# Kernel tuning notes

Hardware: AMD Instinct MI355X
Metric: run time of the kernel (lower is better)

The kernel has to match this reference:

```python
import jax, jax.numpy as jnp
import numpy as np

N = 12288   # nodes
E = 393216  # edges (avg degree 32)
D = 128     # input feature dim


def setup_inputs() -> dict:
    key = jax.random.key(0)
    ks = jax.random.split(key, 8)
    x = jax.random.normal(ks[0], (N, D), dtype=jnp.float32)
    edge_index = jax.random.randint(ks[1], (2, E), 0, N, dtype=jnp.int64)
    def glorot(k, fan_in, fan_out):
        s = jnp.sqrt(6.0 / (fan_in + fan_out)).astype(jnp.float32)
        return jax.random.uniform(k, (fan_in, fan_out), jnp.float32, -s, s)
    W1 = glorot(ks[2], D, 16);  b1 = jnp.zeros((16,), jnp.float32)
    W2 = glorot(ks[3], 16, 8);  b2 = jnp.zeros((8,), jnp.float32)
    Wa = glorot(ks[4], 8, D);   ba = jnp.zeros((D,), jnp.float32)
    Ws = glorot(ks[5], 8, 8);   bs = jnp.zeros((8,), jnp.float32)
    return {"x": x, "edge_index": edge_index,
            "W1": W1, "b1": b1, "W2": W2, "b2": b2,
            "Wa": Wa, "ba": ba, "Ws": Ws, "bs": bs}


def reference(x, edge_index, W1, b1, W2, b2, Wa, ba, Ws, bs):
    n = x.shape[0]
    # GCN symmetric normalization with self-loops (PyG GCNConv defaults)
    loops = jnp.arange(n, dtype=edge_index.dtype)
    src = jnp.concatenate([edge_index[0], loops])
    dst = jnp.concatenate([edge_index[1], loops])
    deg = jax.ops.segment_sum(jnp.ones_like(dst, dtype=x.dtype), dst, num_segments=n)
    dinv = jnp.where(deg > 0, jax.lax.rsqrt(deg), 0.0)
    norm = dinv[src] * dinv[dst]  # [E+N]

    def gcn(h, W, b):
        h = h @ W                                   # [n, out]
        msg = h[src] * norm[:, None]                # gather + scale
        return jax.ops.segment_sum(msg, dst, num_segments=n) + b

    z = jax.nn.relu(gcn(x, W1, b1))
    z = jax.nn.relu(gcn(z, W2, b2))
    x_hat = gcn(z, Wa, ba)
    z_struct = jax.nn.relu(gcn(z, Ws, bs))
    a_hat = z_struct @ z_struct.T                   # [n, n] inner-product decoder
    return (x_hat, a_hat)
```

## Files before the change

kernel.cpp:

```cpp
#include <hip/hip_runtime.h>

typedef float f32x4 __attribute__((ext_vector_type(4)));

#define TPB 256
#define CAP 96

__global__ __launch_bounds__(256) void p1_kernel(
        const float* __restrict__ x, const float* __restrict__ W1,
        const int* __restrict__ src, const int* __restrict__ dst,
        int* __restrict__ cnt, unsigned short* __restrict__ csrd,
        float* __restrict__ h1, int n, int e, int nsb) {
    if ((int)blockIdx.x < nsb) {
        int t = blockIdx.x * blockDim.x + threadIdx.x;
        if (t < e) {
            int d = dst[t];
            int slot = atomicAdd(&cnt[d], 1);
            if (slot < CAP) csrd[(size_t)d * CAP + slot] = (unsigned short)src[t];
        }
        return;
    }
    __shared__ float sW[2048];
    for (int t = threadIdx.x; t < 2048; t += blockDim.x) sW[t] = W1[t];
    __syncthreads();
    int t = ((int)blockIdx.x - nsb) * blockDim.x + threadIdx.x;
    if (t >= n * 16) return;
    int i = t >> 4, j = t & 15;
    const float* xr = x + (size_t)i * 128;
    float s = 0.f;
#pragma unroll
    for (int k = 0; k < 128; k += 4) {
        f32x4 xv = *reinterpret_cast<const f32x4*>(xr + k);
        s = fmaf(xv.x, sW[(k + 0) * 16 + j], s);
        s = fmaf(xv.y, sW[(k + 1) * 16 + j], s);
        s = fmaf(xv.z, sW[(k + 2) * 16 + j], s);
        s = fmaf(xv.w, sW[(k + 3) * 16 + j], s);
    }
    h1[t] = s;
}

__global__ __launch_bounds__(256) void gather_l1(
        const float* __restrict__ h1, const int* __restrict__ cnt,
        const unsigned short* __restrict__ csrd,
        const float* __restrict__ b1, const float* __restrict__ W2,
        float* __restrict__ h2, int n) {
    int wave = (blockIdx.x * blockDim.x + threadIdx.x) >> 6;
    int lane = threadIdx.x & 63;
    if (wave >= n) return;
    const int i = wave;
    const int c = lane & 15;
    const int eg = lane >> 4;
    const unsigned short* row = csrd + (size_t)i * CAP;
    int cn = cnt[i];
    int deg = min(cn, CAP);
    float acc = 0.0f;
    for (int eb = eg; eb < deg; eb += 4) {
        int s = row[eb];
        float ds = rsqrtf((float)(cnt[s] + 1));
        acc = fmaf(ds, h1[(size_t)s * 16 + c], acc);
    }
    acc += __shfl_xor(acc, 16);
    acc += __shfl_xor(acc, 32);
    float di = rsqrtf((float)(cn + 1));
    float z1c = fmaxf(di * fmaf(di, h1[(size_t)i * 16 + c], acc) + b1[c], 0.0f);
    const int j = lane & 7;
    float hj = 0.0f;
#pragma unroll
    for (int k = 0; k < 16; ++k) {
        float v = __shfl(z1c, k);
        hj = fmaf(v, W2[k * 8 + j], hj);
    }
    if (lane < 8) h2[(size_t)i * 8 + lane] = di * hj;
}

__global__ __launch_bounds__(256) void gather_l2(
        const float* __restrict__ h2, const int* __restrict__ cnt,
        const unsigned short* __restrict__ csrd,
        const float* __restrict__ b2, float* __restrict__ z, int n) {
    int wave = (blockIdx.x * blockDim.x + threadIdx.x) >> 6;
    int lane = threadIdx.x & 63;
    if (wave >= n) return;
    const int i = wave;
    const int c = lane & 7;
    const int eg = lane >> 3;
    const unsigned short* row = csrd + (size_t)i * CAP;
    int cn = cnt[i];
    int deg = min(cn, CAP);
    float acc = 0.0f;
    for (int eb = eg; eb < deg; eb += 8) {
        int s = row[eb];
        acc += h2[(size_t)s * 8 + c];
    }
    acc += __shfl_xor(acc, 8);
    acc += __shfl_xor(acc, 16);
    acc += __shfl_xor(acc, 32);
    float di = rsqrtf((float)(cn + 1));
    float zc = fmaxf(di * (acc + h2[(size_t)i * 8 + c]) + b2[c], 0.0f);
    if (lane < 8) z[(size_t)i * 8 + lane] = di * zc;
}

__global__ __launch_bounds__(256) void gather_l34(
        const float* __restrict__ z, const int* __restrict__ cnt,
        const unsigned short* __restrict__ csrd,
        const float* __restrict__ Wa, const float* __restrict__ ba,
        const float* __restrict__ Ws, const float* __restrict__ bs,
        float* __restrict__ xhat, float* __restrict__ zs, int n) {
    int wave = (blockIdx.x * blockDim.x + threadIdx.x) >> 6;
    int lane = threadIdx.x & 63;
    if (wave >= n) return;
    const int i = wave;
    const int c = lane & 7;
    const int eg = lane >> 3;
    const unsigned short* row = csrd + (size_t)i * CAP;
    int cn = cnt[i];
    int deg = min(cn, CAP);
    float acc = 0.0f;
    for (int eb = eg; eb < deg; eb += 8) {
        int s = row[eb];
        acc += z[(size_t)s * 8 + c];
    }
    acc += __shfl_xor(acc, 8);
    acc += __shfl_xor(acc, 16);
    acc += __shfl_xor(acc, 32);
    float di = rsqrtf((float)(cn + 1));
    float agg = di * (acc + z[(size_t)i * 8 + c]);
    float o0 = ba[lane], o1 = ba[lane + 64];
    float zsj = bs[c];
#pragma unroll
    for (int k = 0; k < 8; ++k) {
        float a = __shfl(agg, k);
        o0 = fmaf(a, Wa[k * 128 + lane], o0);
        o1 = fmaf(a, Wa[k * 128 + lane + 64], o1);
        zsj = fmaf(a, Ws[k * 8 + c], zsj);
    }
    __builtin_nontemporal_store(o0, &xhat[(size_t)i * 128 + lane]);
    __builtin_nontemporal_store(o1, &xhat[(size_t)i * 128 + lane + 64]);
    if (lane < 8) zs[(size_t)i * 8 + lane] = fmaxf(zsj, 0.0f);
}

__global__ __launch_bounds__(256) void ahat_kernel(const float* __restrict__ zs,
                                                   float* __restrict__ a, int n) {
    int j0 = blockIdx.x * 1024 + threadIdx.x * 4;
    int i0 = blockIdx.y * 8;
    float zj[4][8];
#pragma unroll
    for (int u = 0; u < 4; ++u) {
        f32x4 lo = *reinterpret_cast<const f32x4*>(&zs[(size_t)(j0 + u) * 8]);
        f32x4 hi = *reinterpret_cast<const f32x4*>(&zs[(size_t)(j0 + u) * 8 + 4]);
        zj[u][0] = lo.x; zj[u][1] = lo.y; zj[u][2] = lo.z; zj[u][3] = lo.w;
        zj[u][4] = hi.x; zj[u][5] = hi.y; zj[u][6] = hi.z; zj[u][7] = hi.w;
    }
    __shared__ float zi[64];
    if (threadIdx.x < 64) zi[threadIdx.x] = zs[(size_t)i0 * 8 + threadIdx.x];
    __syncthreads();
#pragma unroll
    for (int i = 0; i < 8; ++i) {
        float r[4];
#pragma unroll
        for (int u = 0; u < 4; ++u) {
            float s = 0.0f;
#pragma unroll
            for (int k = 0; k < 8; ++k) s = fmaf(zi[i * 8 + k], zj[u][k], s);
            r[u] = s;
        }
        f32x4 v = { r[0], r[1], r[2], r[3] };
        __builtin_nontemporal_store(v, reinterpret_cast<f32x4*>(&a[(size_t)(i0 + i) * n + j0]));
    }
}

extern "C" void kernel_launch(void* const* d_in, const int* in_sizes, int n_in,
                              void* d_out, int out_size, void* d_ws, size_t ws_size,
                              hipStream_t stream) {
    const float* x  = (const float*)d_in[0];
    const int*   ei = (const int*)d_in[1];
    const float* W1 = (const float*)d_in[2];
    const float* b1 = (const float*)d_in[3];
    const float* W2 = (const float*)d_in[4];
    const float* b2 = (const float*)d_in[5];
    const float* Wa = (const float*)d_in[6];
    const float* ba = (const float*)d_in[7];
    const float* Ws = (const float*)d_in[8];
    const float* bs = (const float*)d_in[9];

    const int n = in_sizes[0] / 128;
    const int e = in_sizes[1] / 2;
    const int* srcp = ei;
    const int* dstp = ei + e;

    float* xhat = (float*)d_out;
    float* ahat = xhat + (size_t)n * 128;

    int*            cnt  = (int*)d_ws;
    unsigned short* csrd = (unsigned short*)(cnt + n);
    float*          h1   = (float*)(csrd + (size_t)n * CAP);
    float*          h2   = h1 + (size_t)16 * n;
    float*          zbuf = h2 + (size_t)8 * n;
    float*          zs   = zbuf + (size_t)8 * n;

    auto cdiv = [](long long a, long long b) { return (int)((a + b - 1) / b); };

    hipMemsetAsync(cnt, 0, (size_t)n * sizeof(int), stream);

    const int nsb = cdiv(e, TPB);
    const int nmb = cdiv((long long)n * 16, TPB);
    p1_kernel<<<nsb + nmb, TPB, 0, stream>>>(x, W1, srcp, dstp, cnt, csrd, h1, n, e, nsb);

    gather_l1<<<cdiv((long long)n * 64, TPB), TPB, 0, stream>>>(h1, cnt, csrd, b1, W2, h2, n);
    gather_l2<<<cdiv((long long)n * 64, TPB), TPB, 0, stream>>>(h2, cnt, csrd, b2, zbuf, n);
    gather_l34<<<cdiv((long long)n * 64, TPB), TPB, 0, stream>>>(zbuf, cnt, csrd,
                                                                 Wa, ba, Ws, bs, xhat, zs, n);

    dim3 agrid((n + 1023) / 1024, (n + 7) / 8);
    ahat_kernel<<<agrid, 256, 0, stream>>>(zs, ahat, n);
}
```

Before: 151.6 us.

## Move x_hat projection out of last gather into the a_hat launch

The last gather kernel now writes only the aggregated 8-dim features and z_struct. The 128-wide x_hat projection moves into the a_hat kernel as extra leading blocks, so the x_hat stores share a launch with the large a_hat write stream. The intent is to shorten the latency-bound gather kernel and overlap the x_hat writes with the bandwidth-bound a_hat output. In exchange it adds an intermediate agg buffer round trip and a flattened 1D grid with div/mod indexing.

```diff
diff --git a/kernel.cpp b/kernel.cpp
--- a/kernel.cpp
+++ b/kernel.cpp
@@ -98,12 +98,11 @@
     if (lane < 8) z[(size_t)i * 8 + lane] = di * zc;
 }
 
-__global__ __launch_bounds__(256) void gather_l34(
+__global__ __launch_bounds__(256) void gather_zs(
         const float* __restrict__ z, const int* __restrict__ cnt,
         const unsigned short* __restrict__ csrd,
-        const float* __restrict__ Wa, const float* __restrict__ ba,
         const float* __restrict__ Ws, const float* __restrict__ bs,
-        float* __restrict__ xhat, float* __restrict__ zs, int n) {
+        float* __restrict__ agg, float* __restrict__ zs, int n) {
     int wave = (blockIdx.x * blockDim.x + threadIdx.x) >> 6;
     int lane = threadIdx.x & 63;
     if (wave >= n) return;
@@ -122,25 +121,42 @@
     acc += __shfl_xor(acc, 16);
     acc += __shfl_xor(acc, 32);
     float di = rsqrtf((float)(cn + 1));
-    float agg = di * (acc + z[(size_t)i * 8 + c]);
-    float o0 = ba[lane], o1 = ba[lane + 64];
+    float a_c = di * (acc + z[(size_t)i * 8 + c]);
+    if (lane < 8) agg[(size_t)i * 8 + lane] = a_c;
     float zsj = bs[c];
 #pragma unroll
     for (int k = 0; k < 8; ++k) {
-        float a = __shfl(agg, k);
-        o0 = fmaf(a, Wa[k * 128 + lane], o0);
-        o1 = fmaf(a, Wa[k * 128 + lane + 64], o1);
+        float a = __shfl(a_c, k);
         zsj = fmaf(a, Ws[k * 8 + c], zsj);
     }
-    __builtin_nontemporal_store(o0, &xhat[(size_t)i * 128 + lane]);
-    __builtin_nontemporal_store(o1, &xhat[(size_t)i * 128 + lane + 64]);
     if (lane < 8) zs[(size_t)i * 8 + lane] = fmaxf(zsj, 0.0f);
 }
 
-__global__ __launch_bounds__(256) void ahat_kernel(const float* __restrict__ zs,
-                                                   float* __restrict__ a, int n) {
-    int j0 = blockIdx.x * 1024 + threadIdx.x * 4;
-    int i0 = blockIdx.y * 8;
+__global__ __launch_bounds__(256) void ahat_fused(
+        const float* __restrict__ zs, const float* __restrict__ agg,
+        const float* __restrict__ Wa, const float* __restrict__ ba,
+        float* __restrict__ xhat, float* __restrict__ a, int n, int nxb, int nbx) {
+    if ((int)blockIdx.x < nxb) {
+        int wave = (blockIdx.x * blockDim.x + threadIdx.x) >> 6;
+        int lane = threadIdx.x & 63;
+        if (wave >= n) return;
+        float a_c = agg[(size_t)wave * 8 + (lane & 7)];
+        float o0 = ba[lane], o1 = ba[lane + 64];
+#pragma unroll
+        for (int k = 0; k < 8; ++k) {
+            float av = __shfl(a_c, k);
+            o0 = fmaf(av, Wa[k * 128 + lane], o0);
+            o1 = fmaf(av, Wa[k * 128 + lane + 64], o1);
+        }
+        __builtin_nontemporal_store(o0, &xhat[(size_t)wave * 128 + lane]);
+        __builtin_nontemporal_store(o1, &xhat[(size_t)wave * 128 + lane + 64]);
+        return;
+    }
+    int idx = (int)blockIdx.x - nxb;
+    int bx = idx % nbx;
+    int by = idx / nbx;
+    int j0 = bx * 1024 + threadIdx.x * 4;
+    int i0 = by * 8;
     float zj[4][8];
 #pragma unroll
     for (int u = 0; u < 4; ++u) {
@@ -195,6 +211,7 @@
     float*          h2   = h1 + (size_t)16 * n;
     float*          zbuf = h2 + (size_t)8 * n;
     float*          zs   = zbuf + (size_t)8 * n;
+    float*          agg  = zs + (size_t)8 * n;
 
     auto cdiv = [](long long a, long long b) { return (int)((a + b - 1) / b); };
 
@@ -206,9 +223,10 @@
 
     gather_l1<<<cdiv((long long)n * 64, TPB), TPB, 0, stream>>>(h1, cnt, csrd, b1, W2, h2, n);
     gather_l2<<<cdiv((long long)n * 64, TPB), TPB, 0, stream>>>(h2, cnt, csrd, b2, zbuf, n);
-    gather_l34<<<cdiv((long long)n * 64, TPB), TPB, 0, stream>>>(zbuf, cnt, csrd,
-                                                                 Wa, ba, Ws, bs, xhat, zs, n);
-
-    dim3 agrid((n + 1023) / 1024, (n + 7) / 8);
-    ahat_kernel<<<agrid, 256, 0, stream>>>(zs, ahat, n);
-}
+    gather_zs<<<cdiv((long long)n * 64, TPB), TPB, 0, stream>>>(zbuf, cnt, csrd, Ws, bs, agg, zs, n);
+
+    const int nxb = cdiv((long long)n * 64, TPB);
+    const int nbx = cdiv(n, 1024);
+    const int nab = nbx * cdiv(n, 8);
+    ahat_fused<<<nxb + nab, TPB, 0, stream>>>(zs, agg, Wa, ba, xhat, ahat, n, nxb, nbx);
+}
```

Result: no change. 153.0 us (+0.9%).
